# Optimization experiments

Measured on AMD Instinct MI355X. Metric: run time of the kernel, lower is better.

Reference implementation:

```python
import jax, jax.numpy as jnp
import numpy as np
import math

HEADS = 32
DIM_HEAD = 64
DM = HEADS * DIM_HEAD  # 2048
B, S = 2, 1024
BITS = 3
N_LEVELS = 2 ** BITS
N_GROUPS = (DIM_HEAD + 2) // 3  # 22
PAD = (3 - DIM_HEAD % 3) % 3    # 2
EPS_NORM = 1e-8
EPS_RMS = 1e-6


def _rotors_to_matrices(r):
    # r: (G,4) unit rotors [s, b12, b13, b23] -> (G,3,3) rotation matrices
    s, p, q, rr = r[:, 0], r[:, 1], r[:, 2], r[:, 3]
    s2, p2, q2, r2 = s * s, p * p, q * q, rr * rr
    M = np.zeros((r.shape[0], 3, 3), dtype=np.float32)
    M[:, 0, 0] = s2 - p2 - q2 + r2
    M[:, 0, 1] = 2 * s * p - 2 * q * rr
    M[:, 0, 2] = 2 * s * q + 2 * p * rr
    M[:, 1, 0] = -2 * s * p - 2 * q * rr
    M[:, 1, 1] = s2 - p2 + q2 - r2
    M[:, 1, 2] = 2 * s * rr - 2 * p * q
    M[:, 2, 0] = -2 * s * q + 2 * p * rr
    M[:, 2, 1] = -2 * s * rr - 2 * p * q
    M[:, 2, 2] = s2 + p2 - q2 - r2
    return M


def _make_compressor(seed):
    rng = np.random.default_rng(seed)
    rot = rng.standard_normal((N_GROUPS, 4)).astype(np.float32)
    rot /= np.linalg.norm(rot, axis=-1, keepdims=True)
    M = _rotors_to_matrices(rot)
    sigma = 1.0 / math.sqrt(DIM_HEAD)  # Lloyd-Max for N(0, 1/d)
    C = np.linspace(-3 * sigma, 3 * sigma, N_LEVELS, dtype=np.float32)
    return jnp.asarray(M), jnp.asarray(np.ascontiguousarray(M.transpose(0, 2, 1))), jnp.asarray(C)


def setup_inputs() -> dict:
    key = jax.random.key(0)
    ks = jax.random.split(key, 8)
    x = jax.random.normal(ks[0], (B, S, DM), dtype=jnp.float32)
    w_scale = 0.02
    Wq = jax.random.normal(ks[1], (DM, DM), dtype=jnp.float32) * w_scale
    Wk = jax.random.normal(ks[2], (DM, DM), dtype=jnp.float32) * w_scale
    Wv = jax.random.normal(ks[3], (DM, DM), dtype=jnp.float32) * w_scale
    Wo = jax.random.normal(ks[4], (DM, DM), dtype=jnp.float32) * w_scale
    qn_w = jnp.ones((DM,), dtype=jnp.float32)
    kn_w = jnp.ones((DM,), dtype=jnp.float32)
    Mk, Mtk, Ck = _make_compressor(42)
    Mv, Mtv, Cv = _make_compressor(4200)
    return {"x": x, "Wq": Wq, "Wk": Wk, "Wv": Wv, "Wo": Wo,
            "qn_w": qn_w, "kn_w": kn_w,
            "Mk": Mk, "Mtk": Mtk, "Ck": Ck,
            "Mv": Mv, "Mtv": Mtv, "Cv": Cv}


def _rmsnorm(x, w):
    return x * jax.lax.rsqrt(jnp.mean(x * x, axis=-1, keepdims=True) + EPS_RMS) * w


def _quant_roundtrip(h, M, Mt, C):
    """RotorQuant compress+decompress. h: (B,H,S,Dh) -> (B,H,S,Dh)."""
    norms = jnp.maximum(jnp.linalg.norm(h, axis=-1, keepdims=True), EPS_NORM)
    xu = h / norms
    xu = jnp.pad(xu, ((0, 0), (0, 0), (0, 0), (0, PAD)))
    g = xu.reshape(h.shape[0], h.shape[1], h.shape[2], N_GROUPS, 3)
    rot = jnp.einsum('bhsgi,gij->bhsgj', g, M)
    flat = rot.reshape(h.shape[0], h.shape[1], h.shape[2], N_GROUPS * 3)
    # nearest-centroid quantization (uint8 indices in original)
    idx = jnp.argmin(jnp.abs(flat[..., None] - C), axis=-1)
    deq = C[idx]
    g2 = deq.reshape(h.shape[0], h.shape[1], h.shape[2], N_GROUPS, 3)
    der = jnp.einsum('bhsgi,gij->bhsgj', g2, Mt)
    out = der.reshape(h.shape[0], h.shape[1], h.shape[2], N_GROUPS * 3)[..., :DIM_HEAD]
    return out * norms


def reference(x, Wq, Wk, Wv, Wo, qn_w, kn_w, Mk, Mtk, Ck, Mv, Mtv, Cv):
    b, s, _ = x.shape
    v = x @ Wv
    q = _rmsnorm(x @ Wq, qn_w)
    k = _rmsnorm(x @ Wk, kn_w)
    # split heads -> (B,H,S,Dh)
    qh = q.reshape(b, s, HEADS, DIM_HEAD).transpose(0, 2, 1, 3)
    kh = k.reshape(b, s, HEADS, DIM_HEAD).transpose(0, 2, 1, 3)
    vh = v.reshape(b, s, HEADS, DIM_HEAD).transpose(0, 2, 1, 3)
    # per-head rotor quantization roundtrip of K and V
    kh = _quant_roundtrip(kh, Mk, Mtk, Ck)
    vh = _quant_roundtrip(vh, Mv, Mtv, Cv)
    # scaled dot-product attention
    scores = jnp.einsum('bhqd,bhkd->bhqk', qh, kh) / math.sqrt(DIM_HEAD)
    probs = jax.nn.softmax(scores, axis=-1)
    o = jnp.einsum('bhqk,bhkd->bhqd', probs, vh)
    o = o.transpose(0, 2, 1, 3).reshape(b, s, DM)
    return o @ Wo
```

## Files before the change

### kernel.cpp

```cpp
#include <hip/hip_runtime.h>
#include <hip/hip_bf16.h>
#include <math.h>

#define HEADS 32
#define DIM_HEAD 64
#define DM 2048
#define BATCH 2
#define SEQ 1024
#define NROWS (BATCH * SEQ)
#define NVEC (NROWS * HEADS)
#define N_GROUPS 22
#define N_LEVELS 8
#define EPS_NORM 1e-8f
#define EPS_RMS 1e-6f

typedef float f32x4 __attribute__((ext_vector_type(4)));
typedef __bf16 bf16x8 __attribute__((ext_vector_type(8)));
typedef unsigned short u16x8 __attribute__((ext_vector_type(8)));
typedef unsigned short u16x4 __attribute__((ext_vector_type(4)));

#if __has_builtin(__builtin_amdgcn_exp2f)
#define EXP2F(x) __builtin_amdgcn_exp2f(x)
#else
#define EXP2F(x) exp2f(x)
#endif

__device__ __forceinline__ unsigned short f2bf(float x) {
  union { float f; unsigned u; } v; v.f = x;
  unsigned r = v.u + 0x7fffu + ((v.u >> 16) & 1u);
  return (unsigned short)(r >> 16);
}
__device__ __forceinline__ float bf2f(unsigned short h) {
  union { unsigned u; float f; } v; v.u = ((unsigned)h) << 16;
  return v.f;
}
__device__ __forceinline__ bf16x8 ldfrag(const unsigned short* p) {
  return __builtin_bit_cast(bf16x8, *(const u16x8*)p);
}
#define MFMA16(a, b, c) __builtin_amdgcn_mfma_f32_16x16x32_bf16((a), (b), (c), 0, 0, 0)

__device__ __forceinline__ void stage16(const unsigned short* g, unsigned short* lds) {
  __builtin_amdgcn_global_load_lds(
      (const __attribute__((address_space(1))) unsigned int*)g,
      (__attribute__((address_space(3))) unsigned int*)lds, 16, 0, 0);
}

#define WAITV(N) asm volatile("s_waitcnt vmcnt(" #N ")" ::: "memory")
#define SBARM()  asm volatile("s_barrier" ::: "memory")
#define SFENCE() __builtin_amdgcn_sched_barrier(0)

__global__ __launch_bounds__(256) void split_convert_kernel(
    const float* __restrict__ X, unsigned short* __restrict__ hi,
    unsigned short* __restrict__ lo, int n8) {
  const int i = blockIdx.x * 256 + threadIdx.x;
  if (i >= n8) return;
  const float4 a = ((const float4*)X)[2 * i];
  const float4 b = ((const float4*)X)[2 * i + 1];
  const float v[8] = {a.x, a.y, a.z, a.w, b.x, b.y, b.z, b.w};
  u16x8 h, l;
#pragma unroll
  for (int j = 0; j < 8; ++j) {
    const unsigned short hh = f2bf(v[j]);
    h[j] = hh;
    l[j] = f2bf(v[j] - bf2f(hh));
  }
  ((u16x8*)hi)[i] = h;
  if (lo) ((u16x8*)lo)[i] = l;
}

__global__ __launch_bounds__(256) void transpose_split_batch_kernel(
    const float* __restrict__ W0, const float* __restrict__ W1,
    const float* __restrict__ W2, const float* __restrict__ W3,
    unsigned short* __restrict__ T0h, unsigned short* __restrict__ T1h,
    unsigned short* __restrict__ T1l, unsigned short* __restrict__ T2h,
    unsigned short* __restrict__ T2l, unsigned short* __restrict__ T3h) {
  const int z = blockIdx.z;
  const float* W = (z == 0) ? W0 : (z == 1) ? W1 : (z == 2) ? W2 : W3;
  unsigned short* Th = (z == 0) ? T0h : (z == 1) ? T1h : (z == 2) ? T2h : T3h;
  unsigned short* Tl = (z == 1) ? T1l : (z == 2) ? T2l : nullptr;

  __shared__ float S[64][65];
  const int t = threadIdx.x;
  const int tk = blockIdx.y * 64, tm = blockIdx.x * 64;
  {
    const int r = t >> 2, cs = (t & 3) * 16;
    const float* src = W + (size_t)(tk + r) * DM + tm + cs;
#pragma unroll
    for (int j = 0; j < 16; j += 4) {
      float4 v = *(const float4*)(src + j);
      S[r][cs + j] = v.x; S[r][cs + j + 1] = v.y;
      S[r][cs + j + 2] = v.z; S[r][cs + j + 3] = v.w;
    }
  }
  __syncthreads();
  const int m = t >> 2, ks = (t & 3) * 16;
  u16x8 h0, h1, l0, l1;
#pragma unroll
  for (int j = 0; j < 8; ++j) {
    const float v = S[ks + j][m];
    const unsigned short hh = f2bf(v);
    h0[j] = hh; l0[j] = f2bf(v - bf2f(hh));
  }
#pragma unroll
  for (int j = 0; j < 8; ++j) {
    const float v = S[ks + 8 + j][m];
    const unsigned short hh = f2bf(v);
    h1[j] = hh; l1[j] = f2bf(v - bf2f(hh));
  }
  const size_t o = (size_t)(tm + m) * DM + tk + ks;
  *(u16x8*)&Th[o] = h0; *(u16x8*)&Th[o + 8] = h1;
  if (Tl) { *(u16x8*)&Tl[o] = l0; *(u16x8*)&Tl[o + 8] = l1; }
}

__global__ __launch_bounds__(256) void qkv_gemm_kernel(
    const unsigned short* __restrict__ Ahi, const unsigned short* __restrict__ Alo,
    const unsigned short* __restrict__ Bhi, const unsigned short* __restrict__ Blo,
    float* __restrict__ q, float* __restrict__ k, float* __restrict__ v) {
  __shared__ unsigned short lAhi[128 * 32];
  __shared__ unsigned short lBhi[128 * 32];
  __shared__ unsigned short lAlo[128 * 32];
  __shared__ unsigned short lBlo[128 * 32];

  const int t = threadIdx.x;
  const int lane = t & 63, wave = t >> 6;
  const int wr = wave >> 1, wc = wave & 1;
  const int gm0 = blockIdx.y * 128;
  const int gnc = blockIdx.x * 128;
  const int seg = gnc >> 11;
  const bool split = (seg != 0);
  const int lrsub = lane >> 2;
  const int lcsub = lane & 3;

  f32x4 acc[4][4] = {};

  for (int kt = 0; kt < DM; kt += 32) {
    __syncthreads();
#pragma unroll
    for (int rg = wave; rg < 8; rg += 4) {
      const int lrow = rg * 16 + lrsub;
      const int c = lcsub ^ ((lrow >> 1) & 3);
      const size_t goffA = (size_t)(gm0 + lrow) * DM + kt + c * 8;
      const size_t goffB = (size_t)(gnc + lrow) * DM + kt + c * 8;
      stage16(Ahi + goffA, lAhi + rg * 512);
      stage16(Bhi + goffB, lBhi + rg * 512);
      if (split) {
        stage16(Alo + goffA, lAlo + rg * 512);
        stage16(Blo + goffB, lBlo + rg * 512);
      }
    }
    __syncthreads();

    bf16x8 ah[4], bh[4], al[4], bl[4];
#pragma unroll
    for (int i = 0; i < 4; ++i) {
      const int mrow = wr * 64 + i * 16 + (lane & 15);
      const int offa = mrow * 32 + (((lane >> 4) ^ ((mrow >> 1) & 3)) << 3);
      ah[i] = ldfrag(&lAhi[offa]);
      const int nrow = wc * 64 + i * 16 + (lane & 15);
      const int offb = nrow * 32 + (((lane >> 4) ^ ((nrow >> 1) & 3)) << 3);
      bh[i] = ldfrag(&lBhi[offb]);
      if (split) {
        al[i] = ldfrag(&lAlo[offa]);
        bl[i] = ldfrag(&lBlo[offb]);
      }
    }
#pragma unroll
    for (int i = 0; i < 4; ++i)
#pragma unroll
      for (int j = 0; j < 4; ++j) {
        acc[i][j] = MFMA16(ah[i], bh[j], acc[i][j]);
        if (split) {
          acc[i][j] = MFMA16(ah[i], bl[j], acc[i][j]);
          acc[i][j] = MFMA16(al[i], bh[j], acc[i][j]);
        }
      }
  }

  float* C = (seg == 0) ? q : (seg == 1) ? k : v;
  const int gn0 = gnc & 2047;
#pragma unroll
  for (int i = 0; i < 4; ++i) {
    const int row = gm0 + wr * 64 + i * 16 + ((lane >> 4) << 2);
#pragma unroll
    for (int j = 0; j < 4; ++j) {
      const int col = gn0 + wc * 64 + j * 16 + (lane & 15);
#pragma unroll
      for (int r = 0; r < 4; ++r)
        C[(size_t)(row + r) * DM + col] = acc[i][j][r];
    }
  }
}

__global__ __launch_bounds__(256) void gemm_out_splitk_kernel(
    const unsigned short* __restrict__ Ahi, const unsigned short* __restrict__ Bt,
    float* __restrict__ Cpart) {
  __shared__ unsigned short lAhi[128 * 32];
  __shared__ unsigned short lBhi[128 * 32];

  const int t = threadIdx.x;
  const int lane = t & 63, wave = t >> 6;
  const int wr = wave >> 1, wc = wave & 1;
  const int gm0 = blockIdx.y * 128, gn0 = blockIdx.x * 128;
  const int z = blockIdx.z;
  const int k0 = z * (DM / 2);
  const int lrsub = lane >> 2;
  const int lcsub = lane & 3;

  f32x4 acc[4][4] = {};

  for (int kt = k0; kt < k0 + DM / 2; kt += 32) {
    __syncthreads();
#pragma unroll
    for (int rg = wave; rg < 8; rg += 4) {
      const int lrow = rg * 16 + lrsub;
      const int c = lcsub ^ ((lrow >> 1) & 3);
      stage16(Ahi + (size_t)(gm0 + lrow) * DM + kt + c * 8, lAhi + rg * 512);
      stage16(Bt + (size_t)(gn0 + lrow) * DM + kt + c * 8, lBhi + rg * 512);
    }
    __syncthreads();

    bf16x8 ah[4], bh[4];
#pragma unroll
    for (int i = 0; i < 4; ++i) {
      const int mrow = wr * 64 + i * 16 + (lane & 15);
      ah[i] = ldfrag(&lAhi[mrow * 32 + (((lane >> 4) ^ ((mrow >> 1) & 3)) << 3)]);
      const int nrow = wc * 64 + i * 16 + (lane & 15);
      bh[i] = ldfrag(&lBhi[nrow * 32 + (((lane >> 4) ^ ((nrow >> 1) & 3)) << 3)]);
    }
#pragma unroll
    for (int i = 0; i < 4; ++i)
#pragma unroll
      for (int j = 0; j < 4; ++j)
        acc[i][j] = MFMA16(ah[i], bh[j], acc[i][j]);
  }

  float* C = Cpart + (size_t)z * NROWS * DM;
#pragma unroll
  for (int i = 0; i < 4; ++i) {
    const int row = gm0 + wr * 64 + i * 16 + ((lane >> 4) << 2);
#pragma unroll
    for (int j = 0; j < 4; ++j) {
      const int col = gn0 + wc * 64 + j * 16 + (lane & 15);
#pragma unroll
      for (int r = 0; r < 4; ++r)
        C[(size_t)(row + r) * DM + col] = acc[i][j][r];
    }
  }
}

__global__ __launch_bounds__(256) void add2_f4_kernel(
    const float* __restrict__ a, const float* __restrict__ b,
    float* __restrict__ o, int n4) {
  const int i = blockIdx.x * 256 + threadIdx.x;
  if (i >= n4) return;
  const float4 x = ((const float4*)a)[i];
  const float4 y = ((const float4*)b)[i];
  ((float4*)o)[i] = make_float4(x.x + y.x, x.y + y.y, x.z + y.z, x.w + y.w);
}

__device__ __forceinline__ float wave_sum(float x) {
#pragma unroll
  for (int o = 32; o > 0; o >>= 1) x += __shfl_xor(x, o, 64);
  return x;
}

__global__ __launch_bounds__(256) void rmsnorm_kernel(
    float* __restrict__ y, const float* __restrict__ w) {
  __shared__ float rbuf[4];
  const int row = blockIdx.x;
  float* p = y + (size_t)row * DM;
  const int t = threadIdx.x;
  const int wave = t >> 6, lane = t & 63;

  float ss = 0.f;
#pragma unroll
  for (int c = t; c < DM; c += 256) { float v = p[c]; ss += v * v; }
  ss = wave_sum(ss);
  if (lane == 0) rbuf[wave] = ss;
  __syncthreads();
  ss = rbuf[0] + rbuf[1] + rbuf[2] + rbuf[3];
  const float scale = rsqrtf(ss * (1.0f / DM) + EPS_RMS);
#pragma unroll
  for (int c = t; c < DM; c += 256) p[c] = p[c] * scale * w[c];
}

__global__ __launch_bounds__(256) void rmsnorm_split_kernel(
    const float* __restrict__ y, const float* __restrict__ w,
    unsigned short* __restrict__ hi, unsigned short* __restrict__ lo,
    float post) {
  __shared__ float rbuf[4];
  const int row = blockIdx.x;
  const float* p = y + (size_t)row * DM;
  const int t = threadIdx.x;
  const int wave = t >> 6, lane = t & 63;

  const int c0 = t * 8;
  float4 a = *(const float4*)(p + c0);
  float4 b = *(const float4*)(p + c0 + 4);
  float v[8] = {a.x, a.y, a.z, a.w, b.x, b.y, b.z, b.w};
  float ss = 0.f;
#pragma unroll
  for (int j = 0; j < 8; ++j) ss += v[j] * v[j];
  ss = wave_sum(ss);
  if (lane == 0) rbuf[wave] = ss;
  __syncthreads();
  ss = rbuf[0] + rbuf[1] + rbuf[2] + rbuf[3];
  const float scale = rsqrtf(ss * (1.0f / DM) + EPS_RMS) * post;

  u16x8 hv, lv;
#pragma unroll
  for (int j = 0; j < 8; ++j) {
    const float val = v[j] * scale * w[c0 + j];
    const unsigned short hh = f2bf(val);
    hv[j] = hh; lv[j] = f2bf(val - bf2f(hh));
  }
  *(u16x8*)&hi[(size_t)row * DM + c0] = hv;
  *(u16x8*)&lo[(size_t)row * DM + c0] = lv;
}

__device__ __forceinline__ float qnearest(float v, const float* __restrict__ C) {
  float best = C[0];
  float bd = fabsf(v - C[0]);
#pragma unroll
  for (int i = 1; i < N_LEVELS; ++i) {
    float d = fabsf(v - C[i]);
    if (d < bd) { bd = d; best = C[i]; }
  }
  return best;
}

template <bool WRITE_BF>
__global__ __launch_bounds__(256) void quant_kernel(
    float* __restrict__ kv, const float* __restrict__ M,
    const float* __restrict__ Mt, const float* __restrict__ C,
    unsigned short* __restrict__ hi, unsigned short* __restrict__ lo) {
  const int vec = blockIdx.x * blockDim.x + threadIdx.x;
  if (vec >= NVEC) return;
  float* p = kv + (size_t)vec * DIM_HEAD;

  float h[66];
  float ss = 0.f;
#pragma unroll
  for (int d = 0; d < DIM_HEAD; ++d) { h[d] = p[d]; ss += h[d] * h[d]; }
  float norm = fmaxf(sqrtf(ss), EPS_NORM);
  const float inv = 1.0f / norm;
#pragma unroll
  for (int d = 0; d < DIM_HEAD; ++d) h[d] *= inv;
  h[64] = 0.f; h[65] = 0.f;

#pragma unroll
  for (int g = 0; g < N_GROUPS; ++g) {
    const float* Mg  = M  + g * 9;
    const float* Mtg = Mt + g * 9;
    const float a0 = h[3 * g + 0], a1 = h[3 * g + 1], a2 = h[3 * g + 2];
    const float r0 = a0 * Mg[0] + a1 * Mg[3] + a2 * Mg[6];
    const float r1 = a0 * Mg[1] + a1 * Mg[4] + a2 * Mg[7];
    const float r2 = a0 * Mg[2] + a1 * Mg[5] + a2 * Mg[8];
    const float d0 = qnearest(r0, C);
    const float d1 = qnearest(r1, C);
    const float d2 = qnearest(r2, C);
    h[3 * g + 0] = d0 * Mtg[0] + d1 * Mtg[3] + d2 * Mtg[6];
    h[3 * g + 1] = d0 * Mtg[1] + d1 * Mtg[4] + d2 * Mtg[7];
    h[3 * g + 2] = d0 * Mtg[2] + d1 * Mtg[5] + d2 * Mtg[8];
  }
  if (WRITE_BF) {
#pragma unroll
    for (int g8 = 0; g8 < 8; ++g8) {
      u16x8 hv, lv;
#pragma unroll
      for (int j = 0; j < 8; ++j) {
        const float val = h[g8 * 8 + j] * norm;
        const unsigned short hh = f2bf(val);
        hv[j] = hh; lv[j] = f2bf(val - bf2f(hh));
      }
      *(u16x8*)&hi[(size_t)vec * DIM_HEAD + g8 * 8] = hv;
      *(u16x8*)&lo[(size_t)vec * DIM_HEAD + g8 * 8] = lv;
    }
  } else {
#pragma unroll
    for (int d = 0; d < DIM_HEAD; ++d) p[d] = h[d] * norm;
  }
}

__global__ __launch_bounds__(256) void vt_split_kernel(
    const float* __restrict__ v, unsigned short* __restrict__ hi,
    unsigned short* __restrict__ lo) {
  __shared__ float T[64][65];
  const int s0 = blockIdx.x * 64;
  const int bh = blockIdx.y;
  const int b = bh >> 5, h = bh & 31;
  const int t = threadIdx.x;
  {
    const int sr = t >> 2, dseg = (t & 3) * 16;
    const float* src = v + ((size_t)(b * SEQ + s0 + sr) * DM + h * 64 + dseg);
#pragma unroll
    for (int j = 0; j < 16; j += 4) {
      float4 a = *(const float4*)(src + j);
      T[sr][dseg + j] = a.x; T[sr][dseg + j + 1] = a.y;
      T[sr][dseg + j + 2] = a.z; T[sr][dseg + j + 3] = a.w;
    }
  }
  __syncthreads();
  const int d = t >> 2, sseg = (t & 3) * 16;
  u16x8 h0, h1, l0, l1;
#pragma unroll
  for (int j = 0; j < 8; ++j) {
    const float val = T[sseg + j][d];
    const unsigned short hh = f2bf(val);
    h0[j] = hh; l0[j] = f2bf(val - bf2f(hh));
  }
#pragma unroll
  for (int j = 0; j < 8; ++j) {
    const float val = T[sseg + 8 + j][d];
    const unsigned short hh = f2bf(val);
    h1[j] = hh; l1[j] = f2bf(val - bf2f(hh));
  }
  const size_t o = (size_t)(bh * 64 + d) * SEQ + s0 + sseg;
  *(u16x8*)&hi[o] = h0; *(u16x8*)&hi[o + 8] = h1;
  *(u16x8*)&lo[o] = l0; *(u16x8*)&lo[o + 8] = l1;
}

__global__ __launch_bounds__(256) void attn_mfma_kernel(
    const unsigned short* __restrict__ qhi, const unsigned short* __restrict__ qlo,
    const unsigned short* __restrict__ khi, const unsigned short* __restrict__ klo,
    const unsigned short* __restrict__ vthi, const unsigned short* __restrict__ vtlo,
    unsigned short* __restrict__ ohi) {
  __shared__ unsigned short Ks_h[2][4096], Ks_l[2][4096];
  __shared__ unsigned short Vt_h[2][4096], Vt_l[2][4096];
  __shared__ unsigned int   Ps[4096];

  const int bh = blockIdx.x;
  const int qt = blockIdx.y;
  const int h = bh & 31, b = bh >> 5;
  const int q0 = qt * 64;
  const int t = threadIdx.x, lane = t & 63, w = t >> 6;
  const int quad = lane >> 4, l15 = lane & 15;
  const int srow = lane >> 3, schunk = lane & 7;
  const int pswz = (l15 & 7) << 2;
  unsigned int* Psw = Ps + w * 1024;

  auto stage = [&](const unsigned short* g, int stride, unsigned short* arr) {
#pragma unroll
    for (int it = 0; it < 2; ++it) {
      const int r = w * 16 + it * 8 + srow;
      const int c = schunk ^ (r & 7);
      stage16(g + (size_t)r * stride + c * 8, arr + (w * 16 + it * 8) * 64);
    }
  };

  const unsigned short* gkh = khi + ((size_t)(b * SEQ) * DM + h * 64);
  const unsigned short* gkl = klo + ((size_t)(b * SEQ) * DM + h * 64);
  const unsigned short* gvh = vthi + (size_t)(bh * 64) * SEQ;
  const unsigned short* gvl = vtlo + (size_t)(bh * 64) * SEQ;

  auto stageAll = [&](int kt, int buf) {
    stage(gkh + (size_t)kt * DM, DM, Ks_h[buf]);
    stage(gkl + (size_t)kt * DM, DM, Ks_l[buf]);
    stage(gvh + kt, SEQ, Vt_h[buf]);
    stage(gvl + kt, SEQ, Vt_l[buf]);
  };

  bf16x8 qh[2], ql[2];
  {
    const size_t qrow = (size_t)(b * SEQ + q0 + w * 16 + l15) * DM + h * 64;
#pragma unroll
    for (int ks = 0; ks < 2; ++ks) {
      qh[ks] = ldfrag(&qhi[qrow + ks * 32 + quad * 8]);
      ql[ks] = ldfrag(&qlo[qrow + ks * 32 + quad * 8]);
    }
  }

  f32x4 acc[4] = {};
  float m_prev = -INFINITY;
  float lsum = 0.f;

  stageAll(0, 0);

  for (int tt = 0; tt < 16; ++tt) {
    const int c = tt & 1, n = c ^ 1;
    if (tt < 15) {
      stageAll((tt + 1) * 64, n);
      WAITV(8);
    } else {
      WAITV(0);
    }
    SBARM(); SFENCE();
    const unsigned short* cKh = Ks_h[c];
    const unsigned short* cKl = Ks_l[c];
    const unsigned short* cVh = Vt_h[c];
    const unsigned short* cVl = Vt_l[c];

    f32x4 s[4] = {};
    __builtin_amdgcn_s_setprio(1);
#pragma unroll
    for (int nt = 0; nt < 4; ++nt) {
#pragma unroll
      for (int ks = 0; ks < 2; ++ks) {
        const int row = nt * 16 + l15;
        const int off = row * 64 + (((quad + 4 * ks) ^ (row & 7)) << 3);
        const bf16x8 kh = ldfrag(&cKh[off]);
        const bf16x8 kl = ldfrag(&cKl[off]);
        s[nt] = MFMA16(kh, qh[ks], s[nt]);
        s[nt] = MFMA16(kl, qh[ks], s[nt]);
        s[nt] = MFMA16(kh, ql[ks], s[nt]);
      }
    }
    __builtin_amdgcn_s_setprio(0);

    float mx = s[0][0];
#pragma unroll
    for (int nt = 0; nt < 4; ++nt)
#pragma unroll
      for (int r = 0; r < 4; ++r) mx = fmaxf(mx, s[nt][r]);
    mx = fmaxf(mx, __shfl_xor(mx, 16, 64));
    mx = fmaxf(mx, __shfl_xor(mx, 32, 64));
    const float mn = fmaxf(m_prev, mx);
    const float al = EXP2F(m_prev - mn);
    float rs = 0.f;
#pragma unroll
    for (int nt = 0; nt < 4; ++nt)
#pragma unroll
      for (int r = 0; r < 4; ++r) {
        const float e = EXP2F(s[nt][r] - mn);
        s[nt][r] = e; rs += e;
      }
    rs += __shfl_xor(rs, 16, 64);
    rs += __shfl_xor(rs, 32, 64);
    lsum = lsum * al + rs;
    m_prev = mn;
#pragma unroll
    for (int mt = 0; mt < 4; ++mt) acc[mt] *= al;

#pragma unroll
    for (int nt = 0; nt < 4; ++nt) {
      uint4 pw;
      unsigned int* wp = (unsigned int*)&pw;
#pragma unroll
      for (int r = 0; r < 4; ++r) {
        const unsigned short hh = f2bf(s[nt][r]);
        const unsigned short ll = f2bf(s[nt][r] - bf2f(hh));
        wp[r] = ((unsigned)hh << 16) | (unsigned)ll;
      }
      const int cb = (nt * 16 + quad * 4) ^ pswz;
      *(uint4*)&Psw[l15 * 64 + cb] = pw;
    }

    bf16x8 ph[2], pl[2];
#pragma unroll
    for (int ks = 0; ks < 2; ++ks) {
      const int c0 = (ks * 32 + quad * 8) ^ pswz;
      const int c1 = (ks * 32 + quad * 8 + 4) ^ pswz;
      const uint4 pa = *(const uint4*)&Psw[l15 * 64 + c0];
      const uint4 pb = *(const uint4*)&Psw[l15 * 64 + c1];
      u16x8 hv, lv;
      const unsigned int pw[8] = {pa.x, pa.y, pa.z, pa.w, pb.x, pb.y, pb.z, pb.w};
#pragma unroll
      for (int j = 0; j < 8; ++j) {
        hv[j] = (unsigned short)(pw[j] >> 16);
        lv[j] = (unsigned short)(pw[j] & 0xffffu);
      }
      ph[ks] = __builtin_bit_cast(bf16x8, hv);
      pl[ks] = __builtin_bit_cast(bf16x8, lv);
    }

    __builtin_amdgcn_s_setprio(1);
#pragma unroll
    for (int mt = 0; mt < 4; ++mt) {
#pragma unroll
      for (int ks = 0; ks < 2; ++ks) {
        const int drow = mt * 16 + l15;
        const int offv = drow * 64 + (((quad + 4 * ks) ^ (drow & 7)) << 3);
        const bf16x8 vh = ldfrag(&cVh[offv]);
        const bf16x8 vl = ldfrag(&cVl[offv]);
        acc[mt] = MFMA16(vh, ph[ks], acc[mt]);
        acc[mt] = MFMA16(vh, pl[ks], acc[mt]);
        acc[mt] = MFMA16(vl, ph[ks], acc[mt]);
      }
    }
    __builtin_amdgcn_s_setprio(0);
    SFENCE(); SBARM();
  }

  {
    const float inv = 1.0f / lsum;
    const size_t obase = (size_t)(b * SEQ + q0 + w * 16 + l15) * DM + h * 64;
#pragma unroll
    for (int mt = 0; mt < 4; ++mt) {
      u16x4 ov;
#pragma unroll
      for (int r = 0; r < 4; ++r) ov[r] = f2bf(acc[mt][r] * inv);
      *(u16x4*)&ohi[obase + mt * 16 + quad * 4] = ov;
    }
  }
}

extern "C" void kernel_launch(void* const* d_in, const int* in_sizes, int n_in,
                              void* d_out, int out_size, void* d_ws, size_t ws_size,
                              hipStream_t stream) {
  const float* x    = (const float*)d_in[0];
  const float* Wq   = (const float*)d_in[1];
  const float* Wk   = (const float*)d_in[2];
  const float* Wv   = (const float*)d_in[3];
  const float* Wo   = (const float*)d_in[4];
  const float* qn_w = (const float*)d_in[5];
  const float* kn_w = (const float*)d_in[6];
  const float* Mk   = (const float*)d_in[7];
  const float* Mtk  = (const float*)d_in[8];
  const float* Ck   = (const float*)d_in[9];
  const float* Mv   = (const float*)d_in[10];
  const float* Mtv  = (const float*)d_in[11];
  const float* Cv   = (const float*)d_in[12];
  float* out = (float*)d_out;

  const size_t MBb = 1024ull * 1024ull;
  const size_t SEG = (size_t)DM * DM;
  char* w = (char*)d_ws;
  float* qb = (float*)(w + 0 * MBb);
  float* kb = (float*)(w + 16 * MBb);
  float* vb = (float*)(w + 32 * MBb);
  unsigned short* xhi     = (unsigned short*)(w + 48 * MBb);
  unsigned short* xlo     = (unsigned short*)(w + 56 * MBb);
  unsigned short* wcat_hi = (unsigned short*)(w + 64 * MBb);
  unsigned short* wcat_lo = (unsigned short*)(w + 88 * MBb);
  unsigned short* wot     = (unsigned short*)(w + 112 * MBb);
  unsigned short* q_hi  = wcat_hi;
  unsigned short* k_hi  = wcat_hi + SEG;
  unsigned short* k_lo  = wcat_hi + 2 * SEG;
  unsigned short* q_lo  = wcat_lo;
  unsigned short* vt_hi = wcat_lo + SEG;
  unsigned short* vt_lo = wcat_lo + 2 * SEG;
  unsigned short* o_hi  = xhi;
  float* opart = (float*)(w + 0 * MBb);

  const int n8 = (NROWS * DM) / 8;

  split_convert_kernel<<<n8 / 256, 256, 0, stream>>>(x, xhi, xlo, n8);
  transpose_split_batch_kernel<<<dim3(DM / 64, DM / 64, 4), 256, 0, stream>>>(
      Wq, Wk, Wv, Wo,
      wcat_hi, wcat_hi + SEG, wcat_lo + SEG, wcat_hi + 2 * SEG, wcat_lo + 2 * SEG, wot);

  qkv_gemm_kernel<<<dim3(3 * DM / 128, NROWS / 128), 256, 0, stream>>>(
      xhi, xlo, wcat_hi, wcat_lo, qb, kb, vb);

  rmsnorm_kernel<<<NROWS, 256, 0, stream>>>(kb, kn_w);
  rmsnorm_split_kernel<<<NROWS, 256, 0, stream>>>(
      qb, qn_w, q_hi, q_lo, 0.125f * 1.4426950408889634f);

  quant_kernel<true ><<<NVEC / 256, 256, 0, stream>>>(kb, Mk, Mtk, Ck, k_hi, k_lo);
  quant_kernel<false><<<NVEC / 256, 256, 0, stream>>>(vb, Mv, Mtv, Cv, nullptr, nullptr);
  vt_split_kernel<<<dim3(SEQ / 64, BATCH * HEADS), 256, 0, stream>>>(vb, vt_hi, vt_lo);

  attn_mfma_kernel<<<dim3(BATCH * HEADS, SEQ / 64), 256, 0, stream>>>(
      q_hi, q_lo, k_hi, k_lo, vt_hi, vt_lo, o_hi);

  gemm_out_splitk_kernel<<<dim3(DM / 128, NROWS / 128, 2), 256, 0, stream>>>(
      o_hi, wot, opart);
  add2_f4_kernel<<<(NROWS * DM / 4 + 255) / 256, 256, 0, stream>>>(
      opart, opart + (size_t)NROWS * DM, out, NROWS * DM / 4);
}
```

Baseline: 440.9 us.

## Widen QKV GEMM tile to 128x256 and restructure split-precision MFMA loop

Doubles the N dimension of each QKV GEMM block tile from 128 to 256, so each wave computes a 64x128 sub-tile with 32 accumulators. This gives more A-operand reuse per LDS load and halves the number of blocks. The split-precision (hi/lo) MFMA passes are also reordered into separate phases, so lo fragments are loaded only when needed, and launch_bounds asks for two blocks per CU. In exchange it raises register pressure (128 accumulator floats) and LDS use, and the grid shrinks to 24x16 blocks, which risks lower occupancy or spills.

```diff
diff --git a/kernel.cpp b/kernel.cpp
--- a/kernel.cpp
+++ b/kernel.cpp
@@ -112,78 +112,100 @@
   if (Tl) { *(u16x8*)&Tl[o] = l0; *(u16x8*)&Tl[o + 8] = l1; }
 }
 
-__global__ __launch_bounds__(256) void qkv_gemm_kernel(
+__global__ __launch_bounds__(256, 2) void qkv_gemm_kernel(
     const unsigned short* __restrict__ Ahi, const unsigned short* __restrict__ Alo,
     const unsigned short* __restrict__ Bhi, const unsigned short* __restrict__ Blo,
     float* __restrict__ q, float* __restrict__ k, float* __restrict__ v) {
   __shared__ unsigned short lAhi[128 * 32];
-  __shared__ unsigned short lBhi[128 * 32];
   __shared__ unsigned short lAlo[128 * 32];
-  __shared__ unsigned short lBlo[128 * 32];
+  __shared__ unsigned short lBhi[256 * 32];
+  __shared__ unsigned short lBlo[256 * 32];
 
   const int t = threadIdx.x;
   const int lane = t & 63, wave = t >> 6;
   const int wr = wave >> 1, wc = wave & 1;
   const int gm0 = blockIdx.y * 128;
-  const int gnc = blockIdx.x * 128;
+  const int gnc = blockIdx.x * 256;
   const int seg = gnc >> 11;
   const bool split = (seg != 0);
-  const int lrsub = lane >> 2;
-  const int lcsub = lane & 3;
-
-  f32x4 acc[4][4] = {};
+  const int quad = lane >> 4, l15 = lane & 15;
+  const int srow = lane >> 2, schunk = lane & 3;
+
+  f32x4 acc[4][8] = {};
 
   for (int kt = 0; kt < DM; kt += 32) {
     __syncthreads();
 #pragma unroll
-    for (int rg = wave; rg < 8; rg += 4) {
-      const int lrow = rg * 16 + lrsub;
-      const int c = lcsub ^ ((lrow >> 1) & 3);
-      const size_t goffA = (size_t)(gm0 + lrow) * DM + kt + c * 8;
-      const size_t goffB = (size_t)(gnc + lrow) * DM + kt + c * 8;
-      stage16(Ahi + goffA, lAhi + rg * 512);
-      stage16(Bhi + goffB, lBhi + rg * 512);
-      if (split) {
-        stage16(Alo + goffA, lAlo + rg * 512);
-        stage16(Blo + goffB, lBlo + rg * 512);
-      }
+    for (int it = 0; it < 2; ++it) {
+      const int g = it * 4 + wave;
+      const int r = g * 16 + srow;
+      const int c = schunk ^ ((r >> 1) & 3);
+      const size_t go = (size_t)(gm0 + r) * DM + kt + c * 8;
+      stage16(Ahi + go, lAhi + g * 512);
+      if (split) stage16(Alo + go, lAlo + g * 512);
+    }
+#pragma unroll
+    for (int it = 0; it < 4; ++it) {
+      const int g = it * 4 + wave;
+      const int r = g * 16 + srow;
+      const int c = schunk ^ ((r >> 1) & 3);
+      const size_t go = (size_t)(gnc + r) * DM + kt + c * 8;
+      stage16(Bhi + go, lBhi + g * 512);
+      if (split) stage16(Blo + go, lBlo + g * 512);
     }
     __syncthreads();
 
-    bf16x8 ah[4], bh[4], al[4], bl[4];
+    bf16x8 ah[4], bh[8];
 #pragma unroll
     for (int i = 0; i < 4; ++i) {
-      const int mrow = wr * 64 + i * 16 + (lane & 15);
-      const int offa = mrow * 32 + (((lane >> 4) ^ ((mrow >> 1) & 3)) << 3);
-      ah[i] = ldfrag(&lAhi[offa]);
-      const int nrow = wc * 64 + i * 16 + (lane & 15);
-      const int offb = nrow * 32 + (((lane >> 4) ^ ((nrow >> 1) & 3)) << 3);
-      bh[i] = ldfrag(&lBhi[offb]);
-      if (split) {
-        al[i] = ldfrag(&lAlo[offa]);
-        bl[i] = ldfrag(&lBlo[offb]);
-      }
+      const int row = wr * 64 + i * 16 + l15;
+      ah[i] = ldfrag(&lAhi[row * 32 + ((quad ^ ((row >> 1) & 3)) << 3)]);
+    }
+#pragma unroll
+    for (int j = 0; j < 8; ++j) {
+      const int row = wc * 128 + j * 16 + l15;
+      bh[j] = ldfrag(&lBhi[row * 32 + ((quad ^ ((row >> 1) & 3)) << 3)]);
     }
 #pragma unroll
     for (int i = 0; i < 4; ++i)
 #pragma unroll
-      for (int j = 0; j < 4; ++j) {
+      for (int j = 0; j < 8; ++j)
         acc[i][j] = MFMA16(ah[i], bh[j], acc[i][j]);
-        if (split) {
+
+    if (split) {
+      bf16x8 bl[8];
+#pragma unroll
+      for (int j = 0; j < 8; ++j) {
+        const int row = wc * 128 + j * 16 + l15;
+        bl[j] = ldfrag(&lBlo[row * 32 + ((quad ^ ((row >> 1) & 3)) << 3)]);
+      }
+#pragma unroll
+      for (int i = 0; i < 4; ++i)
+#pragma unroll
+        for (int j = 0; j < 8; ++j)
           acc[i][j] = MFMA16(ah[i], bl[j], acc[i][j]);
+      bf16x8 al[4];
+#pragma unroll
+      for (int i = 0; i < 4; ++i) {
+        const int row = wr * 64 + i * 16 + l15;
+        al[i] = ldfrag(&lAlo[row * 32 + ((quad ^ ((row >> 1) & 3)) << 3)]);
+      }
+#pragma unroll
+      for (int i = 0; i < 4; ++i)
+#pragma unroll
+        for (int j = 0; j < 8; ++j)
           acc[i][j] = MFMA16(al[i], bh[j], acc[i][j]);
-        }
-      }
+    }
   }
 
   float* C = (seg == 0) ? q : (seg == 1) ? k : v;
   const int gn0 = gnc & 2047;
 #pragma unroll
   for (int i = 0; i < 4; ++i) {
-    const int row = gm0 + wr * 64 + i * 16 + ((lane >> 4) << 2);
-#pragma unroll
-    for (int j = 0; j < 4; ++j) {
-      const int col = gn0 + wc * 64 + j * 16 + (lane & 15);
+    const int row = gm0 + wr * 64 + i * 16 + (quad << 2);
+#pragma unroll
+    for (int j = 0; j < 8; ++j) {
+      const int col = gn0 + wc * 128 + j * 16 + l15;
 #pragma unroll
       for (int r = 0; r < 4; ++r)
         C[(size_t)(row + r) * DM + col] = acc[i][j][r];
@@ -639,7 +661,7 @@
       Wq, Wk, Wv, Wo,
       wcat_hi, wcat_hi + SEG, wcat_lo + SEG, wcat_hi + 2 * SEG, wcat_lo + 2 * SEG, wot);
 
-  qkv_gemm_kernel<<<dim3(3 * DM / 128, NROWS / 128), 256, 0, stream>>>(
+  qkv_gemm_kernel<<<dim3(3 * DM / 256, NROWS / 128), 256, 0, stream>>>(
       xhi, xlo, wcat_hi, wcat_lo, qb, kb, vb);
 
   rmsnorm_kernel<<<NROWS, 256, 0, stream>>>(kb, kn_w);
```

New measurement: 446.5 us. Within noise of the previous version (+1.3%).

## Fuse K rmsnorm into quant kernel and V quant into transpose-split

Applied to the files above, without the earlier changes.

Replaces the separate K rmsnorm and K quant kernels with one kernel. In it, each thread owns one 64-wide head vector, and a 32-lane shuffle reduction computes the full-row RMS across the 32 heads. It also merges the V quant pass with the V transpose/bf16 split, staging quantized rows in shared memory before the transposed write. This removes several full-size fp32 read/write passes over K and V and two kernel launches. In exchange it relies on per-thread strided 64-float loads, which coalesce poorly, and a 128-thread block with heavy register use.

```diff
diff --git a/kernel.cpp b/kernel.cpp
--- a/kernel.cpp
+++ b/kernel.cpp
@@ -264,60 +264,6 @@
   return x;
 }
 
-__global__ __launch_bounds__(256) void rmsnorm_kernel(
-    float* __restrict__ y, const float* __restrict__ w) {
-  __shared__ float rbuf[4];
-  const int row = blockIdx.x;
-  float* p = y + (size_t)row * DM;
-  const int t = threadIdx.x;
-  const int wave = t >> 6, lane = t & 63;
-
-  float ss = 0.f;
-#pragma unroll
-  for (int c = t; c < DM; c += 256) { float v = p[c]; ss += v * v; }
-  ss = wave_sum(ss);
-  if (lane == 0) rbuf[wave] = ss;
-  __syncthreads();
-  ss = rbuf[0] + rbuf[1] + rbuf[2] + rbuf[3];
-  const float scale = rsqrtf(ss * (1.0f / DM) + EPS_RMS);
-#pragma unroll
-  for (int c = t; c < DM; c += 256) p[c] = p[c] * scale * w[c];
-}
-
-__global__ __launch_bounds__(256) void rmsnorm_split_kernel(
-    const float* __restrict__ y, const float* __restrict__ w,
-    unsigned short* __restrict__ hi, unsigned short* __restrict__ lo,
-    float post) {
-  __shared__ float rbuf[4];
-  const int row = blockIdx.x;
-  const float* p = y + (size_t)row * DM;
-  const int t = threadIdx.x;
-  const int wave = t >> 6, lane = t & 63;
-
-  const int c0 = t * 8;
-  float4 a = *(const float4*)(p + c0);
-  float4 b = *(const float4*)(p + c0 + 4);
-  float v[8] = {a.x, a.y, a.z, a.w, b.x, b.y, b.z, b.w};
-  float ss = 0.f;
-#pragma unroll
-  for (int j = 0; j < 8; ++j) ss += v[j] * v[j];
-  ss = wave_sum(ss);
-  if (lane == 0) rbuf[wave] = ss;
-  __syncthreads();
-  ss = rbuf[0] + rbuf[1] + rbuf[2] + rbuf[3];
-  const float scale = rsqrtf(ss * (1.0f / DM) + EPS_RMS) * post;
-
-  u16x8 hv, lv;
-#pragma unroll
-  for (int j = 0; j < 8; ++j) {
-    const float val = v[j] * scale * w[c0 + j];
-    const unsigned short hh = f2bf(val);
-    hv[j] = hh; lv[j] = f2bf(val - bf2f(hh));
-  }
-  *(u16x8*)&hi[(size_t)row * DM + c0] = hv;
-  *(u16x8*)&lo[(size_t)row * DM + c0] = lv;
-}
-
 __device__ __forceinline__ float qnearest(float v, const float* __restrict__ C) {
   float best = C[0];
   float bd = fabsf(v - C[0]);
@@ -329,25 +275,9 @@
   return best;
 }
 
-template <bool WRITE_BF>
-__global__ __launch_bounds__(256) void quant_kernel(
-    float* __restrict__ kv, const float* __restrict__ M,
-    const float* __restrict__ Mt, const float* __restrict__ C,
-    unsigned short* __restrict__ hi, unsigned short* __restrict__ lo) {
-  const int vec = blockIdx.x * blockDim.x + threadIdx.x;
-  if (vec >= NVEC) return;
-  float* p = kv + (size_t)vec * DIM_HEAD;
-
-  float h[66];
-  float ss = 0.f;
-#pragma unroll
-  for (int d = 0; d < DIM_HEAD; ++d) { h[d] = p[d]; ss += h[d] * h[d]; }
-  float norm = fmaxf(sqrtf(ss), EPS_NORM);
-  const float inv = 1.0f / norm;
-#pragma unroll
-  for (int d = 0; d < DIM_HEAD; ++d) h[d] *= inv;
-  h[64] = 0.f; h[65] = 0.f;
-
+__device__ __forceinline__ void rotor_roundtrip(
+    float* __restrict__ h, const float* __restrict__ M,
+    const float* __restrict__ Mt, const float* __restrict__ C) {
 #pragma unroll
   for (int g = 0; g < N_GROUPS; ++g) {
     const float* Mg  = M  + g * 9;
@@ -363,61 +293,131 @@
     h[3 * g + 1] = d0 * Mtg[1] + d1 * Mtg[4] + d2 * Mtg[7];
     h[3 * g + 2] = d0 * Mtg[2] + d1 * Mtg[5] + d2 * Mtg[8];
   }
-  if (WRITE_BF) {
-#pragma unroll
-    for (int g8 = 0; g8 < 8; ++g8) {
-      u16x8 hv, lv;
-#pragma unroll
-      for (int j = 0; j < 8; ++j) {
-        const float val = h[g8 * 8 + j] * norm;
-        const unsigned short hh = f2bf(val);
-        hv[j] = hh; lv[j] = f2bf(val - bf2f(hh));
-      }
-      *(u16x8*)&hi[(size_t)vec * DIM_HEAD + g8 * 8] = hv;
-      *(u16x8*)&lo[(size_t)vec * DIM_HEAD + g8 * 8] = lv;
-    }
-  } else {
-#pragma unroll
-    for (int d = 0; d < DIM_HEAD; ++d) p[d] = h[d] * norm;
-  }
-}
-
-__global__ __launch_bounds__(256) void vt_split_kernel(
-    const float* __restrict__ v, unsigned short* __restrict__ hi,
-    unsigned short* __restrict__ lo) {
-  __shared__ float T[64][65];
-  const int s0 = blockIdx.x * 64;
+}
+
+__global__ __launch_bounds__(256) void rmsnorm_split_kernel(
+    const float* __restrict__ y, const float* __restrict__ w,
+    unsigned short* __restrict__ hi, unsigned short* __restrict__ lo,
+    float post) {
+  __shared__ float rbuf[4];
+  const int row = blockIdx.x;
+  const float* p = y + (size_t)row * DM;
+  const int t = threadIdx.x;
+  const int wave = t >> 6, lane = t & 63;
+
+  const int c0 = t * 8;
+  float4 a = *(const float4*)(p + c0);
+  float4 b = *(const float4*)(p + c0 + 4);
+  float v[8] = {a.x, a.y, a.z, a.w, b.x, b.y, b.z, b.w};
+  float ss = 0.f;
+#pragma unroll
+  for (int j = 0; j < 8; ++j) ss += v[j] * v[j];
+  ss = wave_sum(ss);
+  if (lane == 0) rbuf[wave] = ss;
+  __syncthreads();
+  ss = rbuf[0] + rbuf[1] + rbuf[2] + rbuf[3];
+  const float scale = rsqrtf(ss * (1.0f / DM) + EPS_RMS) * post;
+
+  u16x8 hv, lv;
+#pragma unroll
+  for (int j = 0; j < 8; ++j) {
+    const float val = v[j] * scale * w[c0 + j];
+    const unsigned short hh = f2bf(val);
+    hv[j] = hh; lv[j] = f2bf(val - bf2f(hh));
+  }
+  *(u16x8*)&hi[(size_t)row * DM + c0] = hv;
+  *(u16x8*)&lo[(size_t)row * DM + c0] = lv;
+}
+
+__global__ __launch_bounds__(256) void rms_quant_k_kernel(
+    const float* __restrict__ kv, const float* __restrict__ w,
+    const float* __restrict__ M, const float* __restrict__ Mt,
+    const float* __restrict__ C,
+    unsigned short* __restrict__ hi, unsigned short* __restrict__ lo) {
+  const int vec = blockIdx.x * 256 + threadIdx.x;
+  const float* p = kv + (size_t)vec * DIM_HEAD;
+  const float* wv = w + (vec & 31) * 64;
+
+  float h[66];
+  float ssr = 0.f;
+#pragma unroll
+  for (int d = 0; d < DIM_HEAD; ++d) { h[d] = p[d]; ssr += h[d] * h[d]; }
+#pragma unroll
+  for (int off = 1; off < 32; off <<= 1) ssr += __shfl_xor(ssr, off, 32);
+  const float scale = rsqrtf(ssr * (1.0f / DM) + EPS_RMS);
+
+  float ss = 0.f;
+#pragma unroll
+  for (int d = 0; d < DIM_HEAD; ++d) {
+    h[d] = h[d] * scale * wv[d];
+    ss += h[d] * h[d];
+  }
+  const float norm = fmaxf(sqrtf(ss), EPS_NORM);
+  const float inv = 1.0f / norm;
+#pragma unroll
+  for (int d = 0; d < DIM_HEAD; ++d) h[d] *= inv;
+  h[64] = 0.f; h[65] = 0.f;
+
+  rotor_roundtrip(h, M, Mt, C);
+
+#pragma unroll
+  for (int g8 = 0; g8 < 8; ++g8) {
+    u16x8 hv, lv;
+#pragma unroll
+    for (int j = 0; j < 8; ++j) {
+      const float val = h[g8 * 8 + j] * norm;
+      const unsigned short hh = f2bf(val);
+      hv[j] = hh; lv[j] = f2bf(val - bf2f(hh));
+    }
+    *(u16x8*)&hi[(size_t)vec * DIM_HEAD + g8 * 8] = hv;
+    *(u16x8*)&lo[(size_t)vec * DIM_HEAD + g8 * 8] = lv;
+  }
+}
+
+__global__ __launch_bounds__(128) void quant_vt_kernel(
+    const float* __restrict__ vsrc, const float* __restrict__ M,
+    const float* __restrict__ Mt, const float* __restrict__ C,
+    unsigned short* __restrict__ hi, unsigned short* __restrict__ lo) {
+  __shared__ float T[128][65];
   const int bh = blockIdx.y;
-  const int b = bh >> 5, h = bh & 31;
+  const int b = bh >> 5, hh = bh & 31;
+  const int s0 = blockIdx.x * 128;
   const int t = threadIdx.x;
+
   {
-    const int sr = t >> 2, dseg = (t & 3) * 16;
-    const float* src = v + ((size_t)(b * SEQ + s0 + sr) * DM + h * 64 + dseg);
-#pragma unroll
-    for (int j = 0; j < 16; j += 4) {
-      float4 a = *(const float4*)(src + j);
-      T[sr][dseg + j] = a.x; T[sr][dseg + j + 1] = a.y;
-      T[sr][dseg + j + 2] = a.z; T[sr][dseg + j + 3] = a.w;
-    }
+    const int s = s0 + t;
+    const float* p = vsrc + ((size_t)(b * SEQ + s) * DM + hh * 64);
+    float h[66];
+    float ss = 0.f;
+#pragma unroll
+    for (int d = 0; d < DIM_HEAD; ++d) { h[d] = p[d]; ss += h[d] * h[d]; }
+    const float norm = fmaxf(sqrtf(ss), EPS_NORM);
+    const float inv = 1.0f / norm;
+#pragma unroll
+    for (int d = 0; d < DIM_HEAD; ++d) h[d] *= inv;
+    h[64] = 0.f; h[65] = 0.f;
+
+    rotor_roundtrip(h, M, Mt, C);
+
+#pragma unroll
+    for (int d = 0; d < DIM_HEAD; ++d) T[t][d] = h[d] * norm;
   }
   __syncthreads();
-  const int d = t >> 2, sseg = (t & 3) * 16;
-  u16x8 h0, h1, l0, l1;
-#pragma unroll
-  for (int j = 0; j < 8; ++j) {
-    const float val = T[sseg + j][d];
-    const unsigned short hh = f2bf(val);
-    h0[j] = hh; l0[j] = f2bf(val - bf2f(hh));
-  }
-#pragma unroll
-  for (int j = 0; j < 8; ++j) {
-    const float val = T[sseg + 8 + j][d];
-    const unsigned short hh = f2bf(val);
-    h1[j] = hh; l1[j] = f2bf(val - bf2f(hh));
-  }
-  const size_t o = (size_t)(bh * 64 + d) * SEQ + s0 + sseg;
-  *(u16x8*)&hi[o] = h0; *(u16x8*)&hi[o + 8] = h1;
-  *(u16x8*)&lo[o] = l0; *(u16x8*)&lo[o + 8] = l1;
+
+  const int d = t & 63, sh = (t >> 6) * 64;
+  const size_t o = (size_t)(bh * 64 + d) * SEQ + s0 + sh;
+#pragma unroll
+  for (int seg = 0; seg < 8; ++seg) {
+    u16x8 hv, lv;
+#pragma unroll
+    for (int j = 0; j < 8; ++j) {
+      const float val = T[sh + seg * 8 + j][d];
+      const unsigned short hb = f2bf(val);
+      hv[j] = hb; lv[j] = f2bf(val - bf2f(hb));
+    }
+    *(u16x8*)&hi[o + seg * 8] = hv;
+    *(u16x8*)&lo[o + seg * 8] = lv;
+  }
 }
 
 __global__ __launch_bounds__(256) void attn_mfma_kernel(
@@ -537,9 +537,9 @@
       unsigned int* wp = (unsigned int*)&pw;
 #pragma unroll
       for (int r = 0; r < 4; ++r) {
-        const unsigned short hh = f2bf(s[nt][r]);
-        const unsigned short ll = f2bf(s[nt][r] - bf2f(hh));
-        wp[r] = ((unsigned)hh << 16) | (unsigned)ll;
+        const unsigned short hb = f2bf(s[nt][r]);
+        const unsigned short lb = f2bf(s[nt][r] - bf2f(hb));
+        wp[r] = ((unsigned)hb << 16) | (unsigned)lb;
       }
       const int cb = (nt * 16 + quad * 4) ^ pswz;
       *(uint4*)&Psw[l15 * 64 + cb] = pw;
@@ -642,13 +642,12 @@
   qkv_gemm_kernel<<<dim3(3 * DM / 128, NROWS / 128), 256, 0, stream>>>(
       xhi, xlo, wcat_hi, wcat_lo, qb, kb, vb);
 
-  rmsnorm_kernel<<<NROWS, 256, 0, stream>>>(kb, kn_w);
+  rms_quant_k_kernel<<<NVEC / 256, 256, 0, stream>>>(
+      kb, kn_w, Mk, Mtk, Ck, k_hi, k_lo);
   rmsnorm_split_kernel<<<NROWS, 256, 0, stream>>>(
       qb, qn_w, q_hi, q_lo, 0.125f * 1.4426950408889634f);
-
-  quant_kernel<true ><<<NVEC / 256, 256, 0, stream>>>(kb, Mk, Mtk, Ck, k_hi, k_lo);
-  quant_kernel<false><<<NVEC / 256, 256, 0, stream>>>(vb, Mv, Mtv, Cv, nullptr, nullptr);
-  vt_split_kernel<<<dim3(SEQ / 64, BATCH * HEADS), 256, 0, stream>>>(vb, vt_hi, vt_lo);
+  quant_vt_kernel<<<dim3(SEQ / 128, BATCH * HEADS), 128, 0, stream>>>(
+      vb, Mv, Mtv, Cv, vt_hi, vt_lo);
 
   attn_mfma_kernel<<<dim3(BATCH * HEADS, SEQ / 64), 256, 0, stream>>>(
       q_hi, q_lo, k_hi, k_lo, vt_hi, vt_lo, o_hi);
```

Result: faster. 412.0 us (median of 2 runs) (-6.6%).
